# Performance work log

Measured on AMD Instinct MI355X. Metric: run time of the kernel, lower is better.

## Reference

```python
import jax, jax.numpy as jnp
import numpy as np

B, TQ, TK, D = 16, 2048, 2048, 1024


def setup_inputs() -> dict:
    key = jax.random.key(0)
    k1, k2, k3 = jax.random.split(key, 3)
    decoder_output = jax.random.normal(k1, (B, TQ, D), dtype=jnp.float32)
    encoder_output = jax.random.normal(k2, (B, TK, D), dtype=jnp.float32)
    # Dense(rnn_size) params: kernel [D, D] (glorot-like scale), bias [D] (zeros, keras default)
    wa_kernel = jax.random.normal(k3, (D, D), dtype=jnp.float32) * (1.0 / np.sqrt(D))
    wa_bias = jnp.zeros((D,), dtype=jnp.float32)
    return {
        "decoder_output": decoder_output,
        "encoder_output": encoder_output,
        "wa_kernel": wa_kernel,
        "wa_bias": wa_bias,
    }


def reference(decoder_output, encoder_output, wa_kernel, wa_bias):
    # keys = Dense(rnn_size)(encoder_output): [B, TK, D]
    keys = jnp.einsum("bkd,de->bke", encoder_output, wa_kernel) + wa_bias
    # score = decoder_output @ keys^T: [B, TQ, TK]
    score = jnp.einsum("bqd,bkd->bqk", decoder_output, keys)
    # softmax over encoder-time axis (axis=2)
    alignment = jax.nn.softmax(score, axis=2)
    # context = alignment @ encoder_output: [B, TQ, D]
    context = jnp.einsum("bqk,bkd->bqd", alignment, encoder_output)
    return (context, alignment)
```

## Files before the change

kernel.cpp:

```cpp
#include <hip/hip_runtime.h>
#include <math.h>

namespace {

constexpr int Bb = 16;
constexpr int TQ = 2048;
constexpr int TK = 2048;
constexpr int D  = 1024;

typedef __bf16 bf16x8 __attribute__((ext_vector_type(8)));
typedef float  f32x4  __attribute__((ext_vector_type(4)));
typedef unsigned short u16;
typedef unsigned int   u32;
typedef u16 u16x8 __attribute__((ext_vector_type(8)));

typedef __attribute__((address_space(1))) const unsigned char gbyte;
typedef __attribute__((address_space(3))) unsigned char sbyte;

__device__ inline u16 f2bf(float f) {
    u32 u = __builtin_bit_cast(u32, f);
    u += 0x7fffu + ((u >> 16) & 1u);
    return (u16)(u >> 16);
}
__device__ inline float bf2f(u16 h) {
    u32 u = (u32)h << 16;
    return __builtin_bit_cast(float, u);
}
__device__ inline void split1(float f, u16& h, u16& l) {
    h = f2bf(f);
    l = f2bf(f - bf2f(h));
}

__device__ inline void gload16(const void* g, void* l) {
    __builtin_amdgcn_global_load_lds((gbyte*)g, (sbyte*)l, 16, 0, 0);
}


template<bool STAGE, int VM>
__device__ __attribute__((always_inline))
void tile_pair(const char* At, const char* Bt, char* stA, char* stB,
               const u16* a0, const u16* a1, const u16* b0, const u16* b1,
               int aRd, int bRd, f32x4 (&acc)[8][4])
{
    bf16x8 afr[4], bfr[4];
    #pragma unroll
    for (int mt = 0; mt < 4; ++mt)
        afr[mt] = *(const bf16x8*)(At + aRd + mt * 1024);
    #pragma unroll
    for (int nt = 0; nt < 4; ++nt)
        bfr[nt] = *(const bf16x8*)(Bt + bRd + nt * 1024);
    if constexpr (STAGE) {
        gload16(a0, stA);
        gload16(a1, stA + 8192);
    }
    __builtin_amdgcn_s_barrier();
    __builtin_amdgcn_s_setprio(1);
    #pragma unroll
    for (int mt = 0; mt < 4; ++mt)
        #pragma unroll
        for (int nt = 0; nt < 4; ++nt)
            acc[mt][nt] = __builtin_amdgcn_mfma_f32_16x16x32_bf16(
                afr[mt], bfr[nt], acc[mt][nt], 0, 0, 0);
    __builtin_amdgcn_s_setprio(0);
    __builtin_amdgcn_s_barrier();
    #pragma unroll
    for (int mt = 0; mt < 4; ++mt)
        afr[mt] = *(const bf16x8*)(At + aRd + 4096 + mt * 1024);
    if constexpr (STAGE) {
        gload16(b0, stB);
        gload16(b1, stB + 8192);
    }
    __builtin_amdgcn_s_barrier();
    __builtin_amdgcn_s_setprio(1);
    #pragma unroll
    for (int mt = 0; mt < 4; ++mt)
        #pragma unroll
        for (int nt = 0; nt < 4; ++nt)
            acc[4 + mt][nt] = __builtin_amdgcn_mfma_f32_16x16x32_bf16(
                afr[mt], bfr[nt], acc[4 + mt][nt], 0, 0, 0);
    __builtin_amdgcn_s_setprio(0);
    if constexpr (VM == 4)      asm volatile("s_waitcnt vmcnt(4)" ::: "memory");
    else if constexpr (VM == 0) asm volatile("s_waitcnt vmcnt(0)" ::: "memory");
    __builtin_amdgcn_s_barrier();
}

template<int SEGS, int EPI>
__global__ __launch_bounds__(512, 2)
void gemm_nt_pipe(const u16* __restrict__ A, const u16* __restrict__ B,
                  float* __restrict__ Cf, u16* __restrict__ C2,
                  int M, int N, int K,
                  long long sA, long long sB, long long sC)
{
    __shared__ char lds[131072];

    const int tid  = threadIdx.x;
    const int lane = tid & 63;
    const int wave = tid >> 6;
    const int wm   = wave >> 2;
    const int wn   = wave & 3;
    const int lr   = lane & 15;
    const int lq   = lane >> 4;

    const int n0 = blockIdx.x * 256;
    const int m0 = blockIdx.y * 256;
    const int bz = blockIdx.z;

    const int ld = (SEGS == 3) ? 2 * K : K;

    const u16* Ab  = A + (long long)bz * sA;
    const u16* Bbp = B + (long long)bz * sB;

    const int srow = tid >> 2;
    const int scol = (tid & 3) ^ ((tid >> 3) & 3);
    const u16* aS0 = Ab  + (long long)(m0 + srow) * ld + scol * 8;
    const u16* aS1 = aS0 + (long long)128 * ld;
    const u16* bS0 = Bbp + (long long)(n0 + srow) * ld + scol * 8;
    const u16* bS1 = bS0 + (long long)128 * ld;

    char* const stBase = lds;
    const int stW = wave * 1024;

    const int slotswz = (lq ^ ((lr >> 1) & 3)) << 4;
    const int aRd = (wm * 128 + lr) * 64 + slotswz;
    const int bRd = (wn * 64  + lr) * 64 + slotswz;

    f32x4 acc[8][4];
    #pragma unroll
    for (int i = 0; i < 8; ++i)
        #pragma unroll
        for (int j = 0; j < 4; ++j)
            acc[i][j] = (f32x4){0.f, 0.f, 0.f, 0.f};

    const int NT = (SEGS == 3 ? 3 * K : K) / 32;

    int kloc = 0, seg = 0;

    #pragma unroll
    for (int p = 0; p < 2; ++p) {
        const int ao = kloc + ((SEGS == 3 && seg == 2) ? K : 0);
        const int bo = kloc + ((SEGS == 3 && seg == 1) ? K : 0);
        char* tb = stBase + p * 32768;
        gload16(aS0 + ao, tb + stW);
        gload16(aS1 + ao, tb + 8192 + stW);
        gload16(bS0 + bo, tb + 16384 + stW);
        gload16(bS1 + bo, tb + 16384 + 8192 + stW);
        kloc += 32;
        if (SEGS == 3 && kloc == K) { kloc = 0; ++seg; }
    }
    asm volatile("s_waitcnt vmcnt(4)" ::: "memory");
    __builtin_amdgcn_s_barrier();

    for (int t = 0; t < NT - 2; ++t) {
        const char* At = stBase + (t & 3) * 32768;
        char* st = stBase + ((t + 2) & 3) * 32768;
        const int ao = kloc + ((SEGS == 3 && seg == 2) ? K : 0);
        const int bo = kloc + ((SEGS == 3 && seg == 1) ? K : 0);
        tile_pair<true, 4>(At, At + 16384, st + stW, st + 16384 + stW,
                           aS0 + ao, aS1 + ao, bS0 + bo, bS1 + bo,
                           aRd, bRd, acc);
        kloc += 32;
        if (SEGS == 3 && kloc == K) { kloc = 0; ++seg; }
    }
    {
        const char* At = stBase + ((NT - 2) & 3) * 32768;
        tile_pair<false, 0>(At, At + 16384, nullptr, nullptr,
                            nullptr, nullptr, nullptr, nullptr, aRd, bRd, acc);
    }
    {
        const char* At = stBase + ((NT - 1) & 3) * 32768;
        tile_pair<false, -1>(At, At + 16384, nullptr, nullptr,
                             nullptr, nullptr, nullptr, nullptr, aRd, bRd, acc);
    }

    if constexpr (EPI == 0) {
        #pragma unroll
        for (int mt = 0; mt < 8; ++mt) {
            const int row = m0 + wm * 128 + mt * 16 + lq * 4;
            #pragma unroll
            for (int nt = 0; nt < 4; ++nt) {
                const int col = n0 + wn * 64 + nt * 16 + lr;
                #pragma unroll
                for (int rg = 0; rg < 4; ++rg)
                    Cf[(long long)bz * sC + (long long)(row + rg) * N + col] =
                        acc[mt][nt][rg];
            }
        }
    } else {
        #pragma unroll
        for (int mt = 0; mt < 8; ++mt) {
            const int row = m0 + wm * 128 + mt * 16 + lq * 4;
            #pragma unroll
            for (int nt = 0; nt < 4; ++nt) {
                const int col = n0 + wn * 64 + nt * 16 + lr;
                #pragma unroll
                for (int rg = 0; rg < 4; ++rg) {
                    const long long base =
                        (long long)bz * sC + (long long)(row + rg) * (2 * N);
                    u16 h, l;
                    split1(acc[mt][nt][rg], h, l);
                    C2[base + col]     = h;
                    C2[base + N + col] = l;
                }
            }
        }
    }
}

__global__ __launch_bounds__(256)
void split_rows(const float* __restrict__ in, u16* __restrict__ out)
{
    const long long i = (long long)blockIdx.x * 256 + threadIdx.x;
    const long long row = i >> 7;
    const int c = ((int)i & 127) << 3;
    const float* p = in + row * 1024 + c;
    float4 v0 = *(const float4*)p;
    float4 v1 = *(const float4*)(p + 4);
    float x[8] = {v0.x, v0.y, v0.z, v0.w, v1.x, v1.y, v1.z, v1.w};
    u16x8 h, l;
    #pragma unroll
    for (int j = 0; j < 8; ++j) {
        u16 hh, lo;
        split1(x[j], hh, lo);
        h[j] = hh; l[j] = lo;
    }
    u16* q = out + row * 2048 + c;
    *(u16x8*)q = h;
    *(u16x8*)(q + 1024) = l;
}

__global__ __launch_bounds__(256)
void transpose_h(const float* __restrict__ in, u16* __restrict__ outh,
                 int R, int C, long long sIn, long long sOut)
{
    __shared__ float t[32][33];
    const int bz = blockIdx.z;
    const int c0 = blockIdx.x * 32;
    const int r0 = blockIdx.y * 32;
    const float* inb = in + (long long)bz * sIn;
    const int tid = threadIdx.x;
    #pragma unroll
    for (int i = 0; i < 4; ++i) {
        int e = i * 256 + tid;
        int r = e >> 5, c = e & 31;
        t[r][c] = inb[(long long)(r0 + r) * C + c0 + c];
    }
    __syncthreads();
    #pragma unroll
    for (int i = 0; i < 4; ++i) {
        int e = i * 256 + tid;
        int r = e >> 5, c = e & 31;
        outh[(long long)bz * sOut + (long long)(c0 + r) * R + r0 + c] =
            f2bf(t[c][r]);
    }
}

__global__ __launch_bounds__(256)
void transpose_split2(const float* __restrict__ in, u16* __restrict__ out2)
{
    __shared__ float t[32][33];
    const int c0 = blockIdx.x * 32;
    const int r0 = blockIdx.y * 32;
    const int tid = threadIdx.x;
    #pragma unroll
    for (int i = 0; i < 4; ++i) {
        int e = i * 256 + tid;
        int r = e >> 5, c = e & 31;
        t[r][c] = in[(long long)(r0 + r) * D + c0 + c];
    }
    __syncthreads();
    #pragma unroll
    for (int i = 0; i < 4; ++i) {
        int e = i * 256 + tid;
        int r = e >> 5, c = e & 31;
        u16 h, l;
        split1(t[c][r], h, l);
        const long long off = (long long)(c0 + r) * (2 * D) + r0 + c;
        out2[off]     = h;
        out2[off + D] = l;
    }
}

__global__ __launch_bounds__(256)
void softmax_kernel(float* __restrict__ S, u16* __restrict__ Sb)
{
    __shared__ float red[4];
    const long long row = blockIdx.x;
    float* p = S + row * (long long)TK;
    const int tid = threadIdx.x;

    float x[8];
    *(float4*)&x[0] = *(const float4*)(p + tid * 8);
    *(float4*)&x[4] = *(const float4*)(p + tid * 8 + 4);

    float mx = x[0];
    #pragma unroll
    for (int i = 1; i < 8; ++i) mx = fmaxf(mx, x[i]);
    #pragma unroll
    for (int off = 32; off > 0; off >>= 1) mx = fmaxf(mx, __shfl_down(mx, off, 64));
    if ((tid & 63) == 0) red[tid >> 6] = mx;
    __syncthreads();
    mx = fmaxf(fmaxf(red[0], red[1]), fmaxf(red[2], red[3]));
    __syncthreads();

    float s = 0.f;
    #pragma unroll
    for (int i = 0; i < 8; ++i) { x[i] = __expf(x[i] - mx); s += x[i]; }
    #pragma unroll
    for (int off = 32; off > 0; off >>= 1) s += __shfl_down(s, off, 64);
    if ((tid & 63) == 0) red[tid >> 6] = s;
    __syncthreads();
    s = red[0] + red[1] + red[2] + red[3];

    const float inv = 1.f / s;
    #pragma unroll
    for (int i = 0; i < 8; ++i) x[i] *= inv;
    *(float4*)(p + tid * 8)     = *(const float4*)&x[0];
    *(float4*)(p + tid * 8 + 4) = *(const float4*)&x[4];

    u16x8 hb;
    #pragma unroll
    for (int i = 0; i < 8; ++i) hb[i] = f2bf(x[i]);
    *(u16x8*)(Sb + row * (long long)TK + tid * 8) = hb;
}

}

extern "C" void kernel_launch(void* const* d_in, const int* in_sizes, int n_in,
                              void* d_out, int out_size, void* d_ws, size_t ws_size,
                              hipStream_t stream)
{
    typedef long long ll;
    const float* dec = (const float*)d_in[0];
    const float* enc = (const float*)d_in[1];
    const float* W   = (const float*)d_in[2];

    float* out     = (float*)d_out;
    float* context = out;
    float* align   = out + (ll)Bb * TQ * D;

    u16* dec2   = (u16*)d_ws;
    u16* keys2  = dec2 + (ll)Bb * TQ * 2 * D;
    u16* Wt2    = keys2 + (ll)Bb * TK * 2 * D;
    u16* enc2   = (u16*)align;
    u16* encT   = dec2;
    u16* alignb = keys2;

    dim3 blk256(256);
    dim3 blk512(512);

    split_rows<<<dim3(Bb * TQ * D / 8 / 256), blk256, 0, stream>>>(dec, dec2);
    split_rows<<<dim3(Bb * TK * D / 8 / 256), blk256, 0, stream>>>(enc, enc2);
    transpose_split2<<<dim3(D / 32, D / 32, 1), blk256, 0, stream>>>(W, Wt2);
    gemm_nt_pipe<3, 1><<<dim3(D / 256, TK / 256, Bb), blk512, 0, stream>>>(
        enc2, Wt2, nullptr, keys2, TK, D, D,
        (ll)TK * 2 * D, 0LL, (ll)TK * 2 * D);
    gemm_nt_pipe<3, 0><<<dim3(TK / 256, TQ / 256, Bb), blk512, 0, stream>>>(
        dec2, keys2, align, nullptr, TQ, TK, D,
        (ll)TQ * 2 * D, (ll)TK * 2 * D, (ll)TQ * TK);
    transpose_h<<<dim3(D / 32, TK / 32, Bb), blk256, 0, stream>>>(
        enc, encT, TK, D, (ll)TK * D, (ll)D * TK);
    softmax_kernel<<<dim3(Bb * TQ), blk256, 0, stream>>>(align, alignb);
    gemm_nt_pipe<1, 0><<<dim3(D / 256, TQ / 256, Bb), blk512, 0, stream>>>(
        alignb, encT, context, nullptr, TQ, D, TK,
        (ll)TQ * TK, (ll)D * TK, (ll)TQ * D);
}
```

Before: 1.435 ms.

## Restructure GEMM mainloop to 64-wide K tiles with double-buffered LDS

Changes the GEMM main loop from 32-wide K tiles in a 4-slot ring to 64-wide K tiles in a double buffer. Each tile is split into four MFMA phases, with global-to-LDS loads for the next tile interleaved between them and a new XOR swizzle for the 128-byte rows. The goal is fewer barriers and loop iterations per unit of K and more MFMA work between synchronisation points. In exchange, prefetch depth drops to one tile, B fragments stay resident in more registers, and the manual vmcnt/lgkmcnt accounting becomes more fragile.

```diff
diff --git a/kernel.cpp b/kernel.cpp
--- a/kernel.cpp
+++ b/kernel.cpp
@@ -35,52 +35,114 @@
     __builtin_amdgcn_global_load_lds((gbyte*)g, (sbyte*)l, 16, 0, 0);
 }
 
-
-template<bool STAGE, int VM>
+#define MFMA16(d, a, b) d = __builtin_amdgcn_mfma_f32_16x16x32_bf16(a, b, d, 0, 0, 0)
+
+template<bool STAGE>
 __device__ __attribute__((always_inline))
-void tile_pair(const char* At, const char* Bt, char* stA, char* stB,
-               const u16* a0, const u16* a1, const u16* b0, const u16* b1,
-               int aRd, int bRd, f32x4 (&acc)[8][4])
-{
-    bf16x8 afr[4], bfr[4];
-    #pragma unroll
-    for (int mt = 0; mt < 4; ++mt)
-        afr[mt] = *(const bf16x8*)(At + aRd + mt * 1024);
-    #pragma unroll
-    for (int nt = 0; nt < 4; ++nt)
-        bfr[nt] = *(const bf16x8*)(Bt + bRd + nt * 1024);
+void do_tile(const char* buf, char* nA, char* nB,
+             const u16* aP, const u16* bP, long long ld64,
+             int aRd, int bRd, f32x4 (&acc)[8][4])
+{
+    bf16x8 B0,B1,B2,B3,B4,B5,B6,B7, A0,A1,A2,A3;
+
+    A0 = *(const bf16x8*)(buf + aRd);
+    A1 = *(const bf16x8*)(buf + (aRd ^ 64));
+    A2 = *(const bf16x8*)(buf + aRd + 2048);
+    A3 = *(const bf16x8*)(buf + (aRd ^ 64) + 2048);
+    B0 = *(const bf16x8*)(buf + bRd);
+    B1 = *(const bf16x8*)(buf + (bRd ^ 64));
+    B2 = *(const bf16x8*)(buf + bRd + 2048);
+    B3 = *(const bf16x8*)(buf + (bRd ^ 64) + 2048);
+    B4 = *(const bf16x8*)(buf + bRd + 4096);
+    B5 = *(const bf16x8*)(buf + (bRd ^ 64) + 4096);
+    B6 = *(const bf16x8*)(buf + bRd + 6144);
+    B7 = *(const bf16x8*)(buf + (bRd ^ 64) + 6144);
     if constexpr (STAGE) {
-        gload16(a0, stA);
-        gload16(a1, stA + 8192);
-    }
-    __builtin_amdgcn_s_barrier();
+        gload16(aP,              nA);
+        gload16(aP + 2 * ld64,   nA + 16384);
+    }
+    asm volatile("s_waitcnt lgkmcnt(8)" ::: "memory");
+    __builtin_amdgcn_s_barrier();
+    asm volatile("s_waitcnt lgkmcnt(0)" ::: "memory");
     __builtin_amdgcn_s_setprio(1);
-    #pragma unroll
-    for (int mt = 0; mt < 4; ++mt)
-        #pragma unroll
-        for (int nt = 0; nt < 4; ++nt)
-            acc[mt][nt] = __builtin_amdgcn_mfma_f32_16x16x32_bf16(
-                afr[mt], bfr[nt], acc[mt][nt], 0, 0, 0);
+    MFMA16(acc[0][0], A0, B0); MFMA16(acc[0][1], A0, B2);
+    MFMA16(acc[0][2], A0, B4); MFMA16(acc[0][3], A0, B6);
+    MFMA16(acc[1][0], A2, B0); MFMA16(acc[1][1], A2, B2);
+    MFMA16(acc[1][2], A2, B4); MFMA16(acc[1][3], A2, B6);
+    MFMA16(acc[0][0], A1, B1); MFMA16(acc[0][1], A1, B3);
+    MFMA16(acc[0][2], A1, B5); MFMA16(acc[0][3], A1, B7);
+    MFMA16(acc[1][0], A3, B1); MFMA16(acc[1][1], A3, B3);
+    MFMA16(acc[1][2], A3, B5); MFMA16(acc[1][3], A3, B7);
     __builtin_amdgcn_s_setprio(0);
     __builtin_amdgcn_s_barrier();
-    #pragma unroll
-    for (int mt = 0; mt < 4; ++mt)
-        afr[mt] = *(const bf16x8*)(At + aRd + 4096 + mt * 1024);
+
+    A0 = *(const bf16x8*)(buf + aRd + 4096);
+    A1 = *(const bf16x8*)(buf + (aRd ^ 64) + 4096);
+    A2 = *(const bf16x8*)(buf + aRd + 6144);
+    A3 = *(const bf16x8*)(buf + (aRd ^ 64) + 6144);
     if constexpr (STAGE) {
-        gload16(b0, stB);
-        gload16(b1, stB + 8192);
-    }
-    __builtin_amdgcn_s_barrier();
+        gload16(bP,        nB);
+        gload16(bP + ld64, nB + 8192);
+    }
+    __builtin_amdgcn_s_barrier();
+    asm volatile("s_waitcnt lgkmcnt(0)" ::: "memory");
     __builtin_amdgcn_s_setprio(1);
-    #pragma unroll
-    for (int mt = 0; mt < 4; ++mt)
-        #pragma unroll
-        for (int nt = 0; nt < 4; ++nt)
-            acc[4 + mt][nt] = __builtin_amdgcn_mfma_f32_16x16x32_bf16(
-                afr[mt], bfr[nt], acc[4 + mt][nt], 0, 0, 0);
+    MFMA16(acc[2][0], A0, B0); MFMA16(acc[2][1], A0, B2);
+    MFMA16(acc[2][2], A0, B4); MFMA16(acc[2][3], A0, B6);
+    MFMA16(acc[3][0], A2, B0); MFMA16(acc[3][1], A2, B2);
+    MFMA16(acc[3][2], A2, B4); MFMA16(acc[3][3], A2, B6);
+    MFMA16(acc[2][0], A1, B1); MFMA16(acc[2][1], A1, B3);
+    MFMA16(acc[2][2], A1, B5); MFMA16(acc[2][3], A1, B7);
+    MFMA16(acc[3][0], A3, B1); MFMA16(acc[3][1], A3, B3);
+    MFMA16(acc[3][2], A3, B5); MFMA16(acc[3][3], A3, B7);
     __builtin_amdgcn_s_setprio(0);
-    if constexpr (VM == 4)      asm volatile("s_waitcnt vmcnt(4)" ::: "memory");
-    else if constexpr (VM == 0) asm volatile("s_waitcnt vmcnt(0)" ::: "memory");
+    if constexpr (STAGE) asm volatile("s_waitcnt vmcnt(4)" ::: "memory");
+    else                 asm volatile("s_waitcnt vmcnt(0)" ::: "memory");
+    __builtin_amdgcn_s_barrier();
+
+    A0 = *(const bf16x8*)(buf + aRd + 8192);
+    A1 = *(const bf16x8*)(buf + (aRd ^ 64) + 8192);
+    A2 = *(const bf16x8*)(buf + aRd + 10240);
+    A3 = *(const bf16x8*)(buf + (aRd ^ 64) + 10240);
+    if constexpr (STAGE) {
+        gload16(bP + 2 * ld64, nB + 16384);
+        gload16(bP + 3 * ld64, nB + 24576);
+    }
+    __builtin_amdgcn_s_barrier();
+    asm volatile("s_waitcnt lgkmcnt(0)" ::: "memory");
+    __builtin_amdgcn_s_setprio(1);
+    MFMA16(acc[4][0], A0, B0); MFMA16(acc[4][1], A0, B2);
+    MFMA16(acc[4][2], A0, B4); MFMA16(acc[4][3], A0, B6);
+    MFMA16(acc[5][0], A2, B0); MFMA16(acc[5][1], A2, B2);
+    MFMA16(acc[5][2], A2, B4); MFMA16(acc[5][3], A2, B6);
+    MFMA16(acc[4][0], A1, B1); MFMA16(acc[4][1], A1, B3);
+    MFMA16(acc[4][2], A1, B5); MFMA16(acc[4][3], A1, B7);
+    MFMA16(acc[5][0], A3, B1); MFMA16(acc[5][1], A3, B3);
+    MFMA16(acc[5][2], A3, B5); MFMA16(acc[5][3], A3, B7);
+    __builtin_amdgcn_s_setprio(0);
+    __builtin_amdgcn_s_barrier();
+
+    A0 = *(const bf16x8*)(buf + aRd + 12288);
+    A1 = *(const bf16x8*)(buf + (aRd ^ 64) + 12288);
+    A2 = *(const bf16x8*)(buf + aRd + 14336);
+    A3 = *(const bf16x8*)(buf + (aRd ^ 64) + 14336);
+    if constexpr (STAGE) {
+        gload16(aP + ld64,     nA + 8192);
+        gload16(aP + 3 * ld64, nA + 24576);
+    }
+    __builtin_amdgcn_s_barrier();
+    asm volatile("s_waitcnt lgkmcnt(0)" ::: "memory");
+    __builtin_amdgcn_s_setprio(1);
+    MFMA16(acc[6][0], A0, B0); MFMA16(acc[6][1], A0, B2);
+    MFMA16(acc[6][2], A0, B4); MFMA16(acc[6][3], A0, B6);
+    MFMA16(acc[7][0], A2, B0); MFMA16(acc[7][1], A2, B2);
+    MFMA16(acc[7][2], A2, B4); MFMA16(acc[7][3], A2, B6);
+    MFMA16(acc[6][0], A1, B1); MFMA16(acc[6][1], A1, B3);
+    MFMA16(acc[6][2], A1, B5); MFMA16(acc[6][3], A1, B7);
+    MFMA16(acc[7][0], A3, B1); MFMA16(acc[7][1], A3, B3);
+    MFMA16(acc[7][2], A3, B5); MFMA16(acc[7][3], A3, B7);
+    __builtin_amdgcn_s_setprio(0);
+    if constexpr (STAGE) asm volatile("s_waitcnt vmcnt(2)" ::: "memory");
     __builtin_amdgcn_s_barrier();
 }
 
@@ -106,23 +168,19 @@
     const int bz = blockIdx.z;
 
     const int ld = (SEGS == 3) ? 2 * K : K;
+    const long long ld64 = (long long)ld * 64;
 
     const u16* Ab  = A + (long long)bz * sA;
     const u16* Bbp = B + (long long)bz * sB;
 
-    const int srow = tid >> 2;
-    const int scol = (tid & 3) ^ ((tid >> 3) & 3);
-    const u16* aS0 = Ab  + (long long)(m0 + srow) * ld + scol * 8;
-    const u16* aS1 = aS0 + (long long)128 * ld;
-    const u16* bS0 = Bbp + (long long)(n0 + srow) * ld + scol * 8;
-    const u16* bS1 = bS0 + (long long)128 * ld;
-
-    char* const stBase = lds;
-    const int stW = wave * 1024;
-
-    const int slotswz = (lq ^ ((lr >> 1) & 3)) << 4;
-    const int aRd = (wm * 128 + lr) * 64 + slotswz;
-    const int bRd = (wn * 64  + lr) * 64 + slotswz;
+    const int srow  = tid >> 3;
+    const int scol8 = ((tid & 7) ^ (srow & 7)) * 8;
+    const u16* aBase = Ab  + (long long)(m0 + srow) * ld + scol8;
+    const u16* bBase = Bbp + (long long)(n0 + srow) * ld + scol8;
+
+    const int swz = (lq ^ (lr & 7)) << 4;
+    const int aRd = (wm * 128 + lr) * 128 + swz;
+    const int bRd = 32768 + (wn * 64 + lr) * 128 + swz;
 
     f32x4 acc[8][4];
     #pragma unroll
@@ -131,46 +189,36 @@
         for (int j = 0; j < 4; ++j)
             acc[i][j] = (f32x4){0.f, 0.f, 0.f, 0.f};
 
-    const int NT = (SEGS == 3 ? 3 * K : K) / 32;
-
-    int kloc = 0, seg = 0;
-
-    #pragma unroll
-    for (int p = 0; p < 2; ++p) {
-        const int ao = kloc + ((SEGS == 3 && seg == 2) ? K : 0);
-        const int bo = kloc + ((SEGS == 3 && seg == 1) ? K : 0);
-        char* tb = stBase + p * 32768;
-        gload16(aS0 + ao, tb + stW);
-        gload16(aS1 + ao, tb + 8192 + stW);
-        gload16(bS0 + bo, tb + 16384 + stW);
-        gload16(bS1 + bo, tb + 16384 + 8192 + stW);
-        kloc += 32;
-        if (SEGS == 3 && kloc == K) { kloc = 0; ++seg; }
-    }
-    asm volatile("s_waitcnt vmcnt(4)" ::: "memory");
-    __builtin_amdgcn_s_barrier();
-
-    for (int t = 0; t < NT - 2; ++t) {
-        const char* At = stBase + (t & 3) * 32768;
-        char* st = stBase + ((t + 2) & 3) * 32768;
-        const int ao = kloc + ((SEGS == 3 && seg == 2) ? K : 0);
-        const int bo = kloc + ((SEGS == 3 && seg == 1) ? K : 0);
-        tile_pair<true, 4>(At, At + 16384, st + stW, st + 16384 + stW,
-                           aS0 + ao, aS1 + ao, bS0 + bo, bS1 + bo,
-                           aRd, bRd, acc);
-        kloc += 32;
-        if (SEGS == 3 && kloc == K) { kloc = 0; ++seg; }
-    }
+    const int NT = (SEGS == 3 ? 3 * K : K) / 64;
+
     {
-        const char* At = stBase + ((NT - 2) & 3) * 32768;
-        tile_pair<false, 0>(At, At + 16384, nullptr, nullptr,
-                            nullptr, nullptr, nullptr, nullptr, aRd, bRd, acc);
-    }
-    {
-        const char* At = stBase + ((NT - 1) & 3) * 32768;
-        tile_pair<false, -1>(At, At + 16384, nullptr, nullptr,
-                             nullptr, nullptr, nullptr, nullptr, aRd, bRd, acc);
-    }
+        char* nA = lds + tid * 16;
+        char* nB = lds + 32768 + tid * 16;
+        gload16(aBase,            nA);
+        gload16(aBase + 2 * ld64, nA + 16384);
+        gload16(bBase,            nB);
+        gload16(bBase + ld64,     nB + 8192);
+        gload16(bBase + 2 * ld64, nB + 16384);
+        gload16(bBase + 3 * ld64, nB + 24576);
+        gload16(aBase + ld64,     nA + 8192);
+        gload16(aBase + 3 * ld64, nA + 24576);
+    }
+    asm volatile("s_waitcnt vmcnt(2)" ::: "memory");
+    __builtin_amdgcn_s_barrier();
+
+    int kst = 64, seg = 0;
+    for (int t = 0; t < NT - 1; ++t) {
+        if (SEGS == 3 && kst == K) { kst = 0; ++seg; }
+        const u16* aP = aBase + kst + ((SEGS == 3 && seg == 2) ? K : 0);
+        const u16* bP = bBase + kst + ((SEGS == 3 && seg == 1) ? K : 0);
+        const char* cb = lds + (t & 1) * 65536;
+        char* nb = lds + ((t + 1) & 1) * 65536;
+        do_tile<true>(cb, nb + tid * 16, nb + 32768 + tid * 16,
+                      aP, bP, ld64, aRd, bRd, acc);
+        kst += 64;
+    }
+    do_tile<false>(lds + ((NT - 1) & 1) * 65536, lds, lds,
+                   aBase, bBase, ld64, aRd, bRd, acc);
 
     if constexpr (EPI == 0) {
         #pragma unroll
```

Measured after the change: 1.385 ms. -3.5%, faster.

## Deepen GEMM LDS pipeline to three tiles in flight and remap workgroups across XCDs

Applied to the files above, without the earlier changes.

Increases the global-to-LDS prefetch depth from two to three k-tiles within the existing four-slot ring buffer. The vmcnt waits and the epilogue tiles are adjusted to match. It also adds a workgroup index remap that groups consecutive blocks per XCD (stride 8) for better L2 locality, and explicit lgkmcnt waits before the MFMA bursts. Deeper prefetch hides more memory latency, at the cost of an extra tile's worth of outstanding loads.

```diff
diff --git a/kernel.cpp b/kernel.cpp
--- a/kernel.cpp
+++ b/kernel.cpp
@@ -35,51 +35,64 @@
     __builtin_amdgcn_global_load_lds((gbyte*)g, (sbyte*)l, 16, 0, 0);
 }
 
+#define MFMA16(d, a, b) d = __builtin_amdgcn_mfma_f32_16x16x32_bf16(a, b, d, 0, 0, 0)
 
 template<bool STAGE, int VM>
 __device__ __attribute__((always_inline))
-void tile_pair(const char* At, const char* Bt, char* stA, char* stB,
-               const u16* a0, const u16* a1, const u16* b0, const u16* b1,
+void do_tile32(const char* buf, char* sA, char* sB,
+               const u16* aP, const u16* bP, long long ldH,
                int aRd, int bRd, f32x4 (&acc)[8][4])
 {
-    bf16x8 afr[4], bfr[4];
-    #pragma unroll
-    for (int mt = 0; mt < 4; ++mt)
-        afr[mt] = *(const bf16x8*)(At + aRd + mt * 1024);
-    #pragma unroll
-    for (int nt = 0; nt < 4; ++nt)
-        bfr[nt] = *(const bf16x8*)(Bt + bRd + nt * 1024);
+    bf16x8 A0, A1, A2, A3, B0, B1, B2, B3;
+
+    A0 = *(const bf16x8*)(buf + aRd);
+    A1 = *(const bf16x8*)(buf + aRd + 1024);
+    A2 = *(const bf16x8*)(buf + aRd + 2048);
+    A3 = *(const bf16x8*)(buf + aRd + 3072);
+    B0 = *(const bf16x8*)(buf + bRd);
+    B1 = *(const bf16x8*)(buf + bRd + 1024);
+    B2 = *(const bf16x8*)(buf + bRd + 2048);
+    B3 = *(const bf16x8*)(buf + bRd + 3072);
     if constexpr (STAGE) {
-        gload16(a0, stA);
-        gload16(a1, stA + 8192);
-    }
-    __builtin_amdgcn_s_barrier();
+        gload16(aP,       sA);
+        gload16(aP + ldH, sA + 8192);
+    }
+    __builtin_amdgcn_s_barrier();
+    asm volatile("s_waitcnt lgkmcnt(0)" ::: "memory");
     __builtin_amdgcn_s_setprio(1);
-    #pragma unroll
-    for (int mt = 0; mt < 4; ++mt)
-        #pragma unroll
-        for (int nt = 0; nt < 4; ++nt)
-            acc[mt][nt] = __builtin_amdgcn_mfma_f32_16x16x32_bf16(
-                afr[mt], bfr[nt], acc[mt][nt], 0, 0, 0);
+    MFMA16(acc[0][0], A0, B0); MFMA16(acc[0][1], A0, B1);
+    MFMA16(acc[0][2], A0, B2); MFMA16(acc[0][3], A0, B3);
+    MFMA16(acc[1][0], A1, B0); MFMA16(acc[1][1], A1, B1);
+    MFMA16(acc[1][2], A1, B2); MFMA16(acc[1][3], A1, B3);
+    MFMA16(acc[2][0], A2, B0); MFMA16(acc[2][1], A2, B1);
+    MFMA16(acc[2][2], A2, B2); MFMA16(acc[2][3], A2, B3);
+    MFMA16(acc[3][0], A3, B0); MFMA16(acc[3][1], A3, B1);
+    MFMA16(acc[3][2], A3, B2); MFMA16(acc[3][3], A3, B3);
     __builtin_amdgcn_s_setprio(0);
     __builtin_amdgcn_s_barrier();
-    #pragma unroll
-    for (int mt = 0; mt < 4; ++mt)
-        afr[mt] = *(const bf16x8*)(At + aRd + 4096 + mt * 1024);
+
+    A0 = *(const bf16x8*)(buf + aRd + 4096);
+    A1 = *(const bf16x8*)(buf + aRd + 5120);
+    A2 = *(const bf16x8*)(buf + aRd + 6144);
+    A3 = *(const bf16x8*)(buf + aRd + 7168);
     if constexpr (STAGE) {
-        gload16(b0, stB);
-        gload16(b1, stB + 8192);
-    }
-    __builtin_amdgcn_s_barrier();
+        gload16(bP,       sB);
+        gload16(bP + ldH, sB + 8192);
+    }
+    __builtin_amdgcn_s_barrier();
+    asm volatile("s_waitcnt lgkmcnt(0)" ::: "memory");
     __builtin_amdgcn_s_setprio(1);
-    #pragma unroll
-    for (int mt = 0; mt < 4; ++mt)
-        #pragma unroll
-        for (int nt = 0; nt < 4; ++nt)
-            acc[4 + mt][nt] = __builtin_amdgcn_mfma_f32_16x16x32_bf16(
-                afr[mt], bfr[nt], acc[4 + mt][nt], 0, 0, 0);
+    MFMA16(acc[4][0], A0, B0); MFMA16(acc[4][1], A0, B1);
+    MFMA16(acc[4][2], A0, B2); MFMA16(acc[4][3], A0, B3);
+    MFMA16(acc[5][0], A1, B0); MFMA16(acc[5][1], A1, B1);
+    MFMA16(acc[5][2], A1, B2); MFMA16(acc[5][3], A1, B3);
+    MFMA16(acc[6][0], A2, B0); MFMA16(acc[6][1], A2, B1);
+    MFMA16(acc[6][2], A2, B2); MFMA16(acc[6][3], A2, B3);
+    MFMA16(acc[7][0], A3, B0); MFMA16(acc[7][1], A3, B1);
+    MFMA16(acc[7][2], A3, B2); MFMA16(acc[7][3], A3, B3);
     __builtin_amdgcn_s_setprio(0);
-    if constexpr (VM == 4)      asm volatile("s_waitcnt vmcnt(4)" ::: "memory");
+    if constexpr (VM == 8)      asm volatile("s_waitcnt vmcnt(8)" ::: "memory");
+    else if constexpr (VM == 4) asm volatile("s_waitcnt vmcnt(4)" ::: "memory");
     else if constexpr (VM == 0) asm volatile("s_waitcnt vmcnt(0)" ::: "memory");
     __builtin_amdgcn_s_barrier();
 }
@@ -92,6 +105,17 @@
                   long long sA, long long sB, long long sC)
 {
     __shared__ char lds[131072];
+
+    int bx = blockIdx.x, by = blockIdx.y, bz = blockIdx.z;
+    {
+        const int gx = gridDim.x, gy = gridDim.y;
+        const int nwg = gx * gy * (int)gridDim.z;
+        const int flat = bx + gx * (by + gy * bz);
+        const int q = nwg >> 3;
+        int s = (flat & 7) * q + (flat >> 3);
+        bx = s % gx; s /= gx;
+        by = s % gy; bz = s / gy;
+    }
 
     const int tid  = threadIdx.x;
     const int lane = tid & 63;
@@ -101,28 +125,23 @@
     const int lr   = lane & 15;
     const int lq   = lane >> 4;
 
-    const int n0 = blockIdx.x * 256;
-    const int m0 = blockIdx.y * 256;
-    const int bz = blockIdx.z;
+    const int n0 = bx * 256;
+    const int m0 = by * 256;
 
     const int ld = (SEGS == 3) ? 2 * K : K;
+    const long long ldH = (long long)128 * ld;
 
     const u16* Ab  = A + (long long)bz * sA;
     const u16* Bbp = B + (long long)bz * sB;
 
     const int srow = tid >> 2;
-    const int scol = (tid & 3) ^ ((tid >> 3) & 3);
-    const u16* aS0 = Ab  + (long long)(m0 + srow) * ld + scol * 8;
-    const u16* aS1 = aS0 + (long long)128 * ld;
-    const u16* bS0 = Bbp + (long long)(n0 + srow) * ld + scol * 8;
-    const u16* bS1 = bS0 + (long long)128 * ld;
-
-    char* const stBase = lds;
-    const int stW = wave * 1024;
-
-    const int slotswz = (lq ^ ((lr >> 1) & 3)) << 4;
-    const int aRd = (wm * 128 + lr) * 64 + slotswz;
-    const int bRd = (wn * 64  + lr) * 64 + slotswz;
+    const int scol = ((tid & 3) ^ ((tid >> 3) & 3)) * 8;
+    const u16* aS = Ab  + (long long)(m0 + srow) * ld + scol;
+    const u16* bS = Bbp + (long long)(n0 + srow) * ld + scol;
+
+    const int swz = (lq ^ ((lr >> 1) & 3)) << 4;
+    const int aRd = (wm * 128 + lr) * 64 + swz;
+    const int bRd = 16384 + (wn * 64 + lr) * 64 + swz;
 
     f32x4 acc[8][4];
     #pragma unroll
@@ -133,44 +152,38 @@
 
     const int NT = (SEGS == 3 ? 3 * K : K) / 32;
 
-    int kloc = 0, seg = 0;
-
-    #pragma unroll
-    for (int p = 0; p < 2; ++p) {
-        const int ao = kloc + ((SEGS == 3 && seg == 2) ? K : 0);
-        const int bo = kloc + ((SEGS == 3 && seg == 1) ? K : 0);
-        char* tb = stBase + p * 32768;
-        gload16(aS0 + ao, tb + stW);
-        gload16(aS1 + ao, tb + 8192 + stW);
-        gload16(bS0 + bo, tb + 16384 + stW);
-        gload16(bS1 + bo, tb + 16384 + 8192 + stW);
-        kloc += 32;
-        if (SEGS == 3 && kloc == K) { kloc = 0; ++seg; }
-    }
-    asm volatile("s_waitcnt vmcnt(4)" ::: "memory");
-    __builtin_amdgcn_s_barrier();
-
-    for (int t = 0; t < NT - 2; ++t) {
-        const char* At = stBase + (t & 3) * 32768;
-        char* st = stBase + ((t + 2) & 3) * 32768;
-        const int ao = kloc + ((SEGS == 3 && seg == 2) ? K : 0);
-        const int bo = kloc + ((SEGS == 3 && seg == 1) ? K : 0);
-        tile_pair<true, 4>(At, At + 16384, st + stW, st + 16384 + stW,
-                           aS0 + ao, aS1 + ao, bS0 + bo, bS1 + bo,
-                           aRd, bRd, acc);
-        kloc += 32;
-        if (SEGS == 3 && kloc == K) { kloc = 0; ++seg; }
-    }
-    {
-        const char* At = stBase + ((NT - 2) & 3) * 32768;
-        tile_pair<false, 0>(At, At + 16384, nullptr, nullptr,
-                            nullptr, nullptr, nullptr, nullptr, aRd, bRd, acc);
-    }
-    {
-        const char* At = stBase + ((NT - 1) & 3) * 32768;
-        tile_pair<false, -1>(At, At + 16384, nullptr, nullptr,
-                             nullptr, nullptr, nullptr, nullptr, aRd, bRd, acc);
-    }
+    int kst = 0, seg = 0;
+    #pragma unroll
+    for (int p = 0; p < 3; ++p) {
+        const int ao = kst + ((SEGS == 3 && seg == 2) ? K : 0);
+        const int bo = kst + ((SEGS == 3 && seg == 1) ? K : 0);
+        char* sl = lds + p * 32768;
+        gload16(aS + ao,       sl + tid * 16);
+        gload16(aS + ao + ldH, sl + 8192 + tid * 16);
+        gload16(bS + bo,       sl + 16384 + tid * 16);
+        gload16(bS + bo + ldH, sl + 24576 + tid * 16);
+        kst += 32;
+        if (SEGS == 3 && kst == K) { kst = 0; ++seg; }
+    }
+    asm volatile("s_waitcnt vmcnt(8)" ::: "memory");
+    __builtin_amdgcn_s_barrier();
+
+    for (int t = 0; t < NT - 3; ++t) {
+        const int ao = kst + ((SEGS == 3 && seg == 2) ? K : 0);
+        const int bo = kst + ((SEGS == 3 && seg == 1) ? K : 0);
+        const char* cb = lds + (t & 3) * 32768;
+        char* nb = lds + ((t + 3) & 3) * 32768;
+        do_tile32<true, 8>(cb, nb + tid * 16, nb + 16384 + tid * 16,
+                           aS + ao, bS + bo, ldH, aRd, bRd, acc);
+        kst += 32;
+        if (SEGS == 3 && kst == K) { kst = 0; ++seg; }
+    }
+    do_tile32<false, 4>(lds + ((NT - 3) & 3) * 32768, nullptr, nullptr,
+                        aS, bS, ldH, aRd, bRd, acc);
+    do_tile32<false, 0>(lds + ((NT - 2) & 3) * 32768, nullptr, nullptr,
+                        aS, bS, ldH, aRd, bRd, acc);
+    do_tile32<false, -1>(lds + ((NT - 1) & 3) * 32768, nullptr, nullptr,
+                         aS, bS, ldH, aRd, bRd, acc);
 
     if constexpr (EPI == 0) {
         #pragma unroll
```

Measured after the change: 1.440 ms. No clear change (+0.3%).
